# Kernel tuning notes

Hardware: AMD Instinct MI355X
Metric: run time of the kernel (lower is better)

The kernel has to match this reference:

```python
import jax, jax.numpy as jnp
import numpy as np

D_MODEL = 1024
NUM_HEADS = 16
HEAD_DIM = D_MODEL // NUM_HEADS
SCALE = HEAD_DIM ** -0.5
LN_EPS = 1e-5
Q_EPS = 1e-5


def bit_quant(W):
    # BitNet b1.58 ternary weight quantization with straight-through estimator.
    gamma = jnp.mean(jnp.abs(W))
    Wq = jnp.clip(jnp.round(W / (gamma + Q_EPS)), -1.0, 1.0) * gamma
    return W + jax.lax.stop_gradient(Wq - W)


def layer_norm(x, gamma, beta):
    mu = jnp.mean(x, axis=-1, keepdims=True)
    var = jnp.mean(jnp.square(x - mu), axis=-1, keepdims=True)
    return (x - mu) * jax.lax.rsqrt(var + LN_EPS) * gamma + beta


def setup_inputs() -> dict:
    key = jax.random.key(0)
    ks = jax.random.split(key, 8)
    B, T, T_ctx, C = 4, 1024, 2048, D_MODEL
    w_std = C ** -0.5
    return {
        "x": jax.random.normal(ks[0], (B, T, C), jnp.float32),
        "context": jax.random.normal(ks[1], (B, T_ctx, C), jnp.float32),
        "Wq": jax.random.normal(ks[2], (C, C), jnp.float32) * w_std,
        "bq": jnp.zeros((C,), jnp.float32),
        "Wk": jax.random.normal(ks[3], (C, C), jnp.float32) * w_std,
        "bk": jnp.zeros((C,), jnp.float32),
        "Wv": jax.random.normal(ks[4], (C, C), jnp.float32) * w_std,
        "bv": jnp.zeros((C,), jnp.float32),
        "Wo": jax.random.normal(ks[5], (C, C), jnp.float32) * w_std,
        "bo": jnp.zeros((C,), jnp.float32),
        "ln_gamma": jnp.ones((C,), jnp.float32),
        "ln_beta": jnp.zeros((C,), jnp.float32),
    }


def reference(x, context, Wq, bq, Wk, bk, Wv, bv, Wo, bo, ln_gamma, ln_beta):
    B, T, C = x.shape
    T_ctx = context.shape[1]
    residual = x
    xn = layer_norm(x, ln_gamma, ln_beta)
    # BitNet-quantized projections (torch Linear: y = x @ W.T + b)
    q = xn @ bit_quant(Wq).T + bq                      # [B,T,C]
    k = context @ bit_quant(Wk).T + bk                 # [B,T_ctx,C]
    v = context @ bit_quant(Wv).T + bv                 # [B,T_ctx,C]
    q = q.reshape(B, T, NUM_HEADS, HEAD_DIM)
    k = k.reshape(B, T_ctx, NUM_HEADS, HEAD_DIM)
    v = v.reshape(B, T_ctx, NUM_HEADS, HEAD_DIM)
    scores = jnp.einsum("bqhd,bkhd->bhqk", q, k) * SCALE   # [B,H,T,T_ctx]
    probs = jax.nn.softmax(scores, axis=-1)
    out = jnp.einsum("bhqk,bkhd->bqhd", probs, v).reshape(B, T, C)
    return residual + (out @ bit_quant(Wo).T + bo)
```

## Files before the change

### kernel.cpp

```cpp
#include <hip/hip_runtime.h>
#include <hip/hip_bf16.h>

typedef __attribute__((ext_vector_type(8))) short s8x;
typedef __attribute__((ext_vector_type(4))) float f4x;
typedef unsigned short u16;
typedef unsigned int u32;

#define T_ 1024
#define TC_ 2048

__device__ __forceinline__ u16 f2bf(float f) {
    u32 u = __float_as_uint(f);
    return (u16)((u + 0x7fffu + ((u >> 16) & 1u)) >> 16);
}

#if defined(__has_builtin)
#if __has_builtin(__builtin_amdgcn_cvt_pk_bf16_f32)
#define HAVE_PK 1
#endif
#endif

__device__ __forceinline__ u32 pack2bf(float a, float b) {
#ifdef HAVE_PK
    typedef __attribute__((ext_vector_type(2))) __bf16 bf2t;
    bf2t r = __builtin_amdgcn_cvt_pk_bf16_f32(a, b);
    u32 u;
    __builtin_memcpy(&u, &r, 4);
    return u;
#else
    return (u32)f2bf(a) | ((u32)f2bf(b) << 16);
#endif
}

__device__ __forceinline__ void gload16(const void* g, void* l) {
    __builtin_amdgcn_global_load_lds((const __attribute__((address_space(1))) u32*)g,
                                     (__attribute__((address_space(3))) u32*)l, 16, 0, 0);
}

__global__ __launch_bounds__(256) void absmean_k(const float* __restrict__ W0, const float* __restrict__ W1,
                                                 const float* __restrict__ W2, const float* __restrict__ W3,
                                                 float* __restrict__ gsum) {
    int wi = blockIdx.y;
    const float* W = (wi == 0) ? W0 : (wi == 1) ? W1 : (wi == 2) ? W2 : W3;
    const int n4 = (1024 * 1024) / 4;
    float s = 0.f;
    int stride = gridDim.x * blockDim.x;
    for (int i = blockIdx.x * blockDim.x + threadIdx.x; i < n4; i += stride) {
        float4 v = ((const float4*)W)[i];
        s += fabsf(v.x) + fabsf(v.y) + fabsf(v.z) + fabsf(v.w);
    }
#pragma unroll
    for (int off = 32; off; off >>= 1) s += __shfl_down(s, off, 64);
    __shared__ float ps[4];
    if ((threadIdx.x & 63) == 0) ps[threadIdx.x >> 6] = s;
    __syncthreads();
    if (threadIdx.x == 0) atomicAdd(gsum + wi, ps[0] + ps[1] + ps[2] + ps[3]);
}

__global__ __launch_bounds__(256) void prep_k(
        const float* __restrict__ x, const float* __restrict__ lng, const float* __restrict__ lnb,
        u16* __restrict__ xn,
        const float* __restrict__ ctx, u16* __restrict__ ctxb,
        const float* __restrict__ W0, const float* __restrict__ W1,
        const float* __restrict__ W2, const float* __restrict__ W3,
        u16* __restrict__ D0, u16* __restrict__ D1, u16* __restrict__ D2, u16* __restrict__ D3,
        const float* __restrict__ gsum) {
    __shared__ float ps[8];
    int bx = blockIdx.x, t = threadIdx.x;
    if (bx < 4096) {
        int row = bx;
        float4 xv = ((const float4*)(x + (long)row * 1024))[t];
        float s = xv.x + xv.y + xv.z + xv.w;
        float s2 = xv.x * xv.x + xv.y * xv.y + xv.z * xv.z + xv.w * xv.w;
#pragma unroll
        for (int off = 32; off; off >>= 1) { s += __shfl_down(s, off, 64); s2 += __shfl_down(s2, off, 64); }
        if ((t & 63) == 0) { ps[t >> 6] = s; ps[4 + (t >> 6)] = s2; }
        __syncthreads();
        float S = ps[0] + ps[1] + ps[2] + ps[3];
        float S2 = ps[4] + ps[5] + ps[6] + ps[7];
        float mu = S * (1.f / 1024.f);
        float var = S2 * (1.f / 1024.f) - mu * mu;
        float rstd = rsqrtf(var + 1e-5f);
        float4 gv = ((const float4*)lng)[t];
        float4 bv = ((const float4*)lnb)[t];
        uint2 o;
        o.x = pack2bf((xv.x - mu) * rstd * gv.x + bv.x, (xv.y - mu) * rstd * gv.y + bv.y);
        o.y = pack2bf((xv.z - mu) * rstd * gv.z + bv.z, (xv.w - mu) * rstd * gv.w + bv.w);
        ((uint2*)(xn + (long)row * 1024))[t] = o;
    } else if (bx < 12288) {
        int i = (bx - 4096) * 256 + t;
        float4 v = ((const float4*)ctx)[i];
        uint2 o = {pack2bf(v.x, v.y), pack2bf(v.z, v.w)};
        ((uint2*)ctxb)[i] = o;
    } else {
        int wi = (bx - 12288) >> 10;
        const float* W = (wi == 0) ? W0 : (wi == 1) ? W1 : (wi == 2) ? W2 : W3;
        u16* D = (wi == 0) ? D0 : (wi == 1) ? D1 : (wi == 2) ? D2 : D3;
        float inv = 1.0f / (gsum[wi] * (1.0f / 1048576.0f) + 1e-5f);
        int i = ((bx - 12288) & 1023) * 256 + t;
        float4 wv = ((const float4*)W)[i];
        uint2 o;
        o.x = pack2bf(fminf(1.f, fmaxf(-1.f, rintf(wv.x * inv))),
                      fminf(1.f, fmaxf(-1.f, rintf(wv.y * inv))));
        o.y = pack2bf(fminf(1.f, fmaxf(-1.f, rintf(wv.z * inv))),
                      fminf(1.f, fmaxf(-1.f, rintf(wv.w * inv))));
        ((uint2*)D)[i] = o;
    }
}

__global__ __launch_bounds__(256) void gemm_fused(
        const u16* __restrict__ xn, const u16* __restrict__ ctxb,
        const u16* __restrict__ wtq, const u16* __restrict__ wtk, const u16* __restrict__ wtv,
        const float* __restrict__ bq, const float* __restrict__ bk, const float* __restrict__ bv,
        const float* __restrict__ gsum,
        u16* __restrict__ qb, u16* __restrict__ kb, u16* __restrict__ vtb) {
    __shared__ __align__(16) char smem[32768];
    int tid = threadIdx.x;
    int w = tid >> 6, l = tid & 63, lq = l & 15, lh = l >> 4;
    int wm = (w >> 1) * 64, wn = (w & 1) * 64;
    int bx = blockIdx.x;
    int prob; const u16 *A, *Wt; const float* bias; int tshift; float sc; int gidx;
    if (bx < 256)      { prob = 0;            A = xn;   Wt = wtq; bias = bq; tshift = 10; sc = 0.125f; gidx = 0; }
    else if (bx < 768) { prob = 1; bx -= 256; A = ctxb; Wt = wtk; bias = bk; tshift = 11; sc = 1.0f;  gidx = 1; }
    else               { prob = 2; bx -= 768; A = ctxb; Wt = wtv; bias = bv; tshift = 11; sc = 1.0f;  gidx = 2; }
    int m0 = (bx >> 3) * 128, n0 = (bx & 7) * 128;
    char* AsB = smem;
    char* BsB = smem + 16384;
    f4x acc[4][4] = {};
    int rb = tid >> 3;
    int cg = (tid & 7) ^ (rb & 7);
    const u16* Ag = A + (long)m0 * 1024 + cg * 8;
    const u16* Bg = Wt + (long)n0 * 1024 + cg * 8;
    for (int k0 = 0; k0 < 1024; k0 += 64) {
        __syncthreads();
#pragma unroll
        for (int i = 0; i < 4; i++) {
            gload16(Ag + (long)(i * 32 + rb) * 1024 + k0, AsB + (i * 256 + tid) * 16);
            gload16(Bg + (long)(i * 32 + rb) * 1024 + k0, BsB + (i * 256 + tid) * 16);
        }
        __syncthreads();
#pragma unroll
        for (int s = 0; s < 2; s++) {
            int sl = (s * 4 + lh) ^ (lq & 7);
            s8x af[4], bfr[4];
#pragma unroll
            for (int i = 0; i < 4; i++) {
                af[i] = *(const s8x*)(AsB + (wm + i * 16 + lq) * 128 + sl * 16);
                bfr[i] = *(const s8x*)(BsB + (wn + i * 16 + lq) * 128 + sl * 16);
            }
#pragma unroll
            for (int i = 0; i < 4; i++)
#pragma unroll
                for (int j = 0; j < 4; j++)
                    acc[i][j] = __builtin_amdgcn_mfma_f32_16x16x32_bf16(af[i], bfr[j], acc[i][j], 0, 0, 0);
        }
    }
    float gamma = gsum[gidx] * (1.0f / 1048576.0f) * sc;
    if (prob < 2) {
        u16* outq = (prob == 0) ? qb : kb;
        int tmask = (1 << tshift) - 1;
#pragma unroll
        for (int i = 0; i < 4; i++) {
            int gr = m0 + wm + i * 16 + lh * 4;
#pragma unroll
            for (int j = 0; j < 4; j++) {
                int gc = n0 + wn + j * 16 + lq;
                float bb = bias[gc] * sc;
                int h = gc >> 6, d = gc & 63;
#pragma unroll
                for (int r = 0; r < 4; r++) {
                    int row = gr + r;
                    int bidx = row >> tshift, tt = row & tmask;
                    outq[((((long)(bidx * 16 + h)) << tshift) + tt) * 64 + d] = f2bf(acc[i][j][r] * gamma + bb);
                }
            }
        }
    } else {
        __syncthreads();
        char* Ct = smem;
#pragma unroll
        for (int i = 0; i < 4; i++) {
            int tt = wm + i * 16 + lh * 4;
#pragma unroll
            for (int j = 0; j < 4; j++) {
                int c = wn + j * 16 + lq;
                float bb = bias[n0 + c];
                uint2 pk;
                pk.x = pack2bf(acc[i][j][0] * gamma + bb, acc[i][j][1] * gamma + bb);
                pk.y = pack2bf(acc[i][j][2] * gamma + bb, acc[i][j][3] * gamma + bb);
                int slot = (tt >> 3) ^ (c & 15);
                *(uint2*)(Ct + c * 256 + slot * 16 + (tt & 7) * 2) = pk;
            }
        }
        __syncthreads();
        int b = m0 >> 11, t0 = m0 & 2047;
#pragma unroll
        for (int it = 0; it < 8; it++) {
            int e = it * 256 + tid;
            int c = e >> 4, ch = e & 15;
            int slot = ch ^ (c & 15);
            s8x v = *(const s8x*)(Ct + c * 256 + slot * 16);
            int gcg = n0 + c;
            int h = gcg >> 6, d = gcg & 63;
            *(s8x*)(vtb + ((long)((b * 16 + h) * 64 + d)) * TC_ + t0 + ch * 8) = v;
        }
    }
}

__global__ __launch_bounds__(256) void gemm_o(const u16* __restrict__ A, const u16* __restrict__ Wt,
                                              const float* __restrict__ bias, const float* __restrict__ gsum,
                                              const float* __restrict__ residual, float* __restrict__ outr) {
    __shared__ __align__(16) char smem[24576];
    int tid = threadIdx.x;
    int w = tid >> 6, l = tid & 63, lq = l & 15, lh = l >> 4;
    int wm = (w >> 1) * 64, wn = (w & 1) * 32;
    int bx = blockIdx.x;
    int m0 = (bx >> 4) * 128, n0 = (bx & 15) * 64;
    char* AsB = smem;
    char* BsB = smem + 16384;
    f4x acc[4][2] = {};
    int rb = tid >> 3;
    int cg = (tid & 7) ^ (rb & 7);
    const u16* Ag = A + (long)m0 * 1024 + cg * 8;
    const u16* Bg = Wt + (long)n0 * 1024 + cg * 8;
    for (int k0 = 0; k0 < 1024; k0 += 64) {
        __syncthreads();
#pragma unroll
        for (int i = 0; i < 4; i++)
            gload16(Ag + (long)(i * 32 + rb) * 1024 + k0, AsB + (i * 256 + tid) * 16);
#pragma unroll
        for (int i = 0; i < 2; i++)
            gload16(Bg + (long)(i * 32 + rb) * 1024 + k0, BsB + (i * 256 + tid) * 16);
        __syncthreads();
#pragma unroll
        for (int s = 0; s < 2; s++) {
            int sl = (s * 4 + lh) ^ (lq & 7);
            s8x af[4], bfr[2];
#pragma unroll
            for (int i = 0; i < 4; i++)
                af[i] = *(const s8x*)(AsB + (wm + i * 16 + lq) * 128 + sl * 16);
#pragma unroll
            for (int j = 0; j < 2; j++)
                bfr[j] = *(const s8x*)(BsB + (wn + j * 16 + lq) * 128 + sl * 16);
#pragma unroll
            for (int i = 0; i < 4; i++)
#pragma unroll
                for (int j = 0; j < 2; j++)
                    acc[i][j] = __builtin_amdgcn_mfma_f32_16x16x32_bf16(af[i], bfr[j], acc[i][j], 0, 0, 0);
        }
    }
    float gamma = gsum[3] * (1.0f / 1048576.0f);
#pragma unroll
    for (int i = 0; i < 4; i++) {
        int gr = m0 + wm + i * 16 + lh * 4;
#pragma unroll
        for (int j = 0; j < 2; j++) {
            int gc = n0 + wn + j * 16 + lq;
            float bb = bias[gc];
#pragma unroll
            for (int r = 0; r < 4; r++) {
                long idx = (long)(gr + r) * 1024 + gc;
                outr[idx] = residual[idx] + acc[i][j][r] * gamma + bb;
            }
        }
    }
}

__global__ __launch_bounds__(256) void attn_k(const u16* __restrict__ qh, const u16* __restrict__ kh,
                                              const u16* __restrict__ vth, u16* __restrict__ attn) {
    __shared__ __align__(16) char smem[51200];
    int tid = threadIdx.x, w = tid >> 6, l = tid & 63, lq = l & 15, lh = l >> 4;
    int bh = blockIdx.x, q0 = blockIdx.y * 128;
    const u16* qp = qh + ((long)bh * T_ + q0) * 64;
    const u16* kp = kh + (long)bh * TC_ * 64;
    const u16* vp = vth + (long)bh * 64 * TC_;
#pragma unroll
    for (int i = 0; i < 4; i++) {
        int cid = i * 256 + tid;
        int r = cid >> 3, c = (cid & 7) ^ (r & 7);
        gload16(qp + r * 64 + c * 8, smem + cid * 16);
    }
    __syncthreads();
    s8x qf[2][2];
#pragma unroll
    for (int nb = 0; nb < 2; nb++)
#pragma unroll
        for (int dh = 0; dh < 2; dh++) {
            int qrow = w * 32 + nb * 16 + lq;
            int ch = (dh * 4 + lh) ^ (qrow & 7);
            qf[nb][dh] = *(const s8x*)(smem + qrow * 128 + ch * 16);
        }
    __syncthreads();
#define STAGE_KV(kt, buf)                                                          \
    {                                                                              \
        char* Kb = smem + (buf) * 16384;                                           \
        char* Vb = Kb + 8192;                                                      \
        _Pragma("unroll") for (int i = 0; i < 2; i++) {                            \
            int cid = i * 256 + tid;                                               \
            int r = cid >> 3, c = (cid & 7) ^ (r & 7);                             \
            gload16(kp + ((kt) * 64 + r) * 64 + c * 8, Kb + cid * 16);             \
            gload16(vp + (long)r * TC_ + (kt) * 64 + c * 8, Vb + cid * 16);        \
        }                                                                          \
    }
    STAGE_KV(0, 0);
    f4x oacc[2][4] = {};
    f4x lrun[2] = {};
    float mrun = -1e30f;
    const s8x ones = {16256, 16256, 16256, 16256, 16256, 16256, 16256, 16256};
    char* Psb = smem + 32768 + w * 4608;
    for (int kt = 0; kt < TC_ / 64; kt++) {
        __syncthreads();
        if (kt + 1 < TC_ / 64) STAGE_KV(kt + 1, (kt + 1) & 1);
        char* Ksb = smem + (kt & 1) * 16384;
        char* Vsb = Ksb + 8192;
        f4x z[2][4];
#pragma unroll
        for (int ni = 0; ni < 4; ni++) {
            int kr = ni * 16 + lq;
            s8x a0 = *(const s8x*)(Ksb + kr * 128 + ((lh) ^ (kr & 7)) * 16);
            s8x a1 = *(const s8x*)(Ksb + kr * 128 + ((4 + lh) ^ (kr & 7)) * 16);
#pragma unroll
            for (int nb = 0; nb < 2; nb++) {
                f4x zz = {0.f, 0.f, 0.f, 0.f};
                zz = __builtin_amdgcn_mfma_f32_16x16x32_bf16(a0, qf[nb][0], zz, 0, 0, 0);
                zz = __builtin_amdgcn_mfma_f32_16x16x32_bf16(a1, qf[nb][1], zz, 0, 0, 0);
                z[nb][ni] = zz;
            }
        }
        float mx = -1e30f;
#pragma unroll
        for (int nb = 0; nb < 2; nb++)
#pragma unroll
            for (int ni = 0; ni < 4; ni++)
#pragma unroll
                for (int r = 0; r < 4; r++) mx = fmaxf(mx, z[nb][ni][r]);
#pragma unroll
        for (int s = 1; s <= 32; s <<= 1) mx = fmaxf(mx, __shfl_xor(mx, s));
        float mn = fmaxf(mrun, mx);
        float al = __expf(mrun - mn);
        mrun = mn;
#pragma unroll
        for (int nb = 0; nb < 2; nb++) {
            int prow = nb * 16 + lq;
#pragma unroll
            for (int ni = 0; ni < 4; ni++) {
                uint2 pk;
                pk.x = pack2bf(__expf(z[nb][ni][0] - mn), __expf(z[nb][ni][1] - mn));
                pk.y = pack2bf(__expf(z[nb][ni][2] - mn), __expf(z[nb][ni][3] - mn));
                *(uint2*)(Psb + prow * 144 + ni * 32 + lh * 8) = pk;
            }
        }
        if (al != 1.0f) {
#pragma unroll
            for (int qb = 0; qb < 2; qb++) {
#pragma unroll
                for (int nd = 0; nd < 4; nd++)
#pragma unroll
                    for (int r = 0; r < 4; r++) oacc[qb][nd][r] *= al;
#pragma unroll
                for (int r = 0; r < 4; r++) lrun[qb][r] *= al;
            }
        }
        s8x vf[4][2];
#pragma unroll
        for (int nd = 0; nd < 4; nd++) {
            int vr = nd * 16 + lq;
            vf[nd][0] = *(const s8x*)(Vsb + vr * 128 + ((lh) ^ (vr & 7)) * 16);
            vf[nd][1] = *(const s8x*)(Vsb + vr * 128 + ((4 + lh) ^ (vr & 7)) * 16);
        }
#pragma unroll
        for (int qb = 0; qb < 2; qb++) {
            int prow = qb * 16 + lq;
            s8x pf0 = *(const s8x*)(Psb + prow * 144 + lh * 16);
            s8x pf1 = *(const s8x*)(Psb + prow * 144 + 64 + lh * 16);
            f4x rs = {0.f, 0.f, 0.f, 0.f};
            rs = __builtin_amdgcn_mfma_f32_16x16x32_bf16(pf0, ones, rs, 0, 0, 0);
            rs = __builtin_amdgcn_mfma_f32_16x16x32_bf16(pf1, ones, rs, 0, 0, 0);
#pragma unroll
            for (int r = 0; r < 4; r++) lrun[qb][r] += rs[r];
#pragma unroll
            for (int nd = 0; nd < 4; nd++) {
                oacc[qb][nd] = __builtin_amdgcn_mfma_f32_16x16x32_bf16(pf0, vf[nd][0], oacc[qb][nd], 0, 0, 0);
                oacc[qb][nd] = __builtin_amdgcn_mfma_f32_16x16x32_bf16(pf1, vf[nd][1], oacc[qb][nd], 0, 0, 0);
            }
        }
    }
    int b = bh >> 4, h = bh & 15;
#pragma unroll
    for (int qb = 0; qb < 2; qb++)
#pragma unroll
        for (int r = 0; r < 4; r++) {
            int q = q0 + w * 32 + qb * 16 + lh * 4 + r;
            float rcp = 1.f / lrun[qb][r];
#pragma unroll
            for (int nd = 0; nd < 4; nd++)
                attn[((long)(b * T_ + q)) * 1024 + h * 64 + nd * 16 + lq] = f2bf(oacc[qb][nd][r] * rcp);
        }
}

extern "C" void kernel_launch(void* const* d_in, const int* in_sizes, int n_in,
                              void* d_out, int out_size, void* d_ws, size_t ws_size,
                              hipStream_t stream) {
    const float* x   = (const float*)d_in[0];
    const float* ctx = (const float*)d_in[1];
    const float* Wq  = (const float*)d_in[2];
    const float* bq  = (const float*)d_in[3];
    const float* Wk  = (const float*)d_in[4];
    const float* bk  = (const float*)d_in[5];
    const float* Wv  = (const float*)d_in[6];
    const float* bv  = (const float*)d_in[7];
    const float* Wo  = (const float*)d_in[8];
    const float* bo  = (const float*)d_in[9];
    const float* lng = (const float*)d_in[10];
    const float* lnb = (const float*)d_in[11];
    float* out = (float*)d_out;

    char* ws = (char*)d_ws;
    float* gsum = (float*)ws;
    size_t off = 256;
    u16* wtq  = (u16*)(ws + off); off += (size_t)1024 * 1024 * 2;
    u16* wtk  = (u16*)(ws + off); off += (size_t)1024 * 1024 * 2;
    u16* wtv  = (u16*)(ws + off); off += (size_t)1024 * 1024 * 2;
    u16* wto  = (u16*)(ws + off); off += (size_t)1024 * 1024 * 2;
    u16* ctxb = (u16*)(ws + off); off += (size_t)8192 * 1024 * 2;
    u16* xn   = (u16*)(ws + off); off += (size_t)4096 * 1024 * 2;
    u16* qb_  = (u16*)(ws + off); off += (size_t)4096 * 1024 * 2;
    u16* kb   = (u16*)(ws + off); off += (size_t)8192 * 1024 * 2;
    u16* vtb  = (u16*)(ws + off); off += (size_t)8192 * 1024 * 2;
    u16* attnb = xn;

    hipMemsetAsync(gsum, 0, 16, stream);
    absmean_k<<<dim3(128, 4), 256, 0, stream>>>(Wq, Wk, Wv, Wo, gsum);
    prep_k<<<16384, 256, 0, stream>>>(x, lng, lnb, xn, ctx, ctxb,
                                      Wq, Wk, Wv, Wo, wtq, wtk, wtv, wto, gsum);
    gemm_fused<<<1280, 256, 0, stream>>>(xn, ctxb, wtq, wtk, wtv, bq, bk, bv, gsum, qb_, kb, vtb);
    attn_k<<<dim3(64, 8), 256, 0, stream>>>(qb_, kb, vtb, attnb);
    gemm_o<<<512, 256, 0, stream>>>(attnb, wto, bo, gsum, x, out);
}
```

Measured before the change: 281.8 us.

## Split attention block across 8 waves with 16 query rows each, use exp2

The attention kernel now launches 512 threads per block. Each of the 8 waves handles 16 query rows instead of 32, which halves per-wave registers and the P scratch and gives the scheduler more waves to hide latency. The K/V staging loads are spread over twice as many threads. The log2(e) factor is folded into the Q projection scale so the softmax can use the native exp2 instruction. In exchange, each K/V tile is reused by fewer query rows per wave, so there are more LDS reads of K and V per unit of MFMA work.

Result: faster. 274.9 us (-2.5%).

```diff
diff --git a/kernel.cpp b/kernel.cpp
--- a/kernel.cpp
+++ b/kernel.cpp
@@ -8,6 +8,7 @@
 
 #define T_ 1024
 #define TC_ 2048
+#define SCLOG2E 0.1803368801111243f
 
 __device__ __forceinline__ u16 f2bf(float f) {
     u32 u = __float_as_uint(f);
@@ -120,7 +121,7 @@
     int wm = (w >> 1) * 64, wn = (w & 1) * 64;
     int bx = blockIdx.x;
     int prob; const u16 *A, *Wt; const float* bias; int tshift; float sc; int gidx;
-    if (bx < 256)      { prob = 0;            A = xn;   Wt = wtq; bias = bq; tshift = 10; sc = 0.125f; gidx = 0; }
+    if (bx < 256)      { prob = 0;            A = xn;   Wt = wtq; bias = bq; tshift = 10; sc = SCLOG2E; gidx = 0; }
     else if (bx < 768) { prob = 1; bx -= 256; A = ctxb; Wt = wtk; bias = bk; tshift = 11; sc = 1.0f;  gidx = 1; }
     else               { prob = 2; bx -= 768; A = ctxb; Wt = wtv; bias = bv; tshift = 11; sc = 1.0f;  gidx = 2; }
     int m0 = (bx >> 3) * 128, n0 = (bx & 7) * 128;
@@ -266,7 +267,7 @@
     }
 }
 
-__global__ __launch_bounds__(256) void attn_k(const u16* __restrict__ qh, const u16* __restrict__ kh,
+__global__ __launch_bounds__(512) void attn_k(const u16* __restrict__ qh, const u16* __restrict__ kh,
                                               const u16* __restrict__ vth, u16* __restrict__ attn) {
     __shared__ __align__(16) char smem[51200];
     int tid = threadIdx.x, w = tid >> 6, l = tid & 63, lq = l & 15, lh = l >> 4;
@@ -275,127 +276,102 @@
     const u16* kp = kh + (long)bh * TC_ * 64;
     const u16* vp = vth + (long)bh * 64 * TC_;
 #pragma unroll
-    for (int i = 0; i < 4; i++) {
-        int cid = i * 256 + tid;
+    for (int i = 0; i < 2; i++) {
+        int cid = i * 512 + tid;
         int r = cid >> 3, c = (cid & 7) ^ (r & 7);
         gload16(qp + r * 64 + c * 8, smem + cid * 16);
     }
     __syncthreads();
-    s8x qf[2][2];
-#pragma unroll
-    for (int nb = 0; nb < 2; nb++)
-#pragma unroll
-        for (int dh = 0; dh < 2; dh++) {
-            int qrow = w * 32 + nb * 16 + lq;
-            int ch = (dh * 4 + lh) ^ (qrow & 7);
-            qf[nb][dh] = *(const s8x*)(smem + qrow * 128 + ch * 16);
-        }
+    s8x qf0, qf1;
+    {
+        int qrow = w * 16 + lq;
+        qf0 = *(const s8x*)(smem + qrow * 128 + ((lh) ^ (qrow & 7)) * 16);
+        qf1 = *(const s8x*)(smem + qrow * 128 + ((4 + lh) ^ (qrow & 7)) * 16);
+    }
     __syncthreads();
-#define STAGE_KV(kt, buf)                                                          \
-    {                                                                              \
-        char* Kb = smem + (buf) * 16384;                                           \
-        char* Vb = Kb + 8192;                                                      \
-        _Pragma("unroll") for (int i = 0; i < 2; i++) {                            \
-            int cid = i * 256 + tid;                                               \
-            int r = cid >> 3, c = (cid & 7) ^ (r & 7);                             \
-            gload16(kp + ((kt) * 64 + r) * 64 + c * 8, Kb + cid * 16);             \
-            gload16(vp + (long)r * TC_ + (kt) * 64 + c * 8, Vb + cid * 16);        \
-        }                                                                          \
+#define STAGE_KV(kt, buf)                                                      \
+    {                                                                          \
+        char* Kb = smem + (buf) * 16384;                                       \
+        char* Vb = Kb + 8192;                                                  \
+        int r = tid >> 3, c = (tid & 7) ^ (r & 7);                             \
+        gload16(kp + ((kt) * 64 + r) * 64 + c * 8, Kb + tid * 16);             \
+        gload16(vp + (long)r * TC_ + (kt) * 64 + c * 8, Vb + tid * 16);        \
     }
     STAGE_KV(0, 0);
-    f4x oacc[2][4] = {};
-    f4x lrun[2] = {};
+    f4x oacc[4] = {};
+    f4x lrun = {};
     float mrun = -1e30f;
     const s8x ones = {16256, 16256, 16256, 16256, 16256, 16256, 16256, 16256};
-    char* Psb = smem + 32768 + w * 4608;
+    char* Psb = smem + 32768 + w * 2304;
     for (int kt = 0; kt < TC_ / 64; kt++) {
         __syncthreads();
         if (kt + 1 < TC_ / 64) STAGE_KV(kt + 1, (kt + 1) & 1);
         char* Ksb = smem + (kt & 1) * 16384;
         char* Vsb = Ksb + 8192;
-        f4x z[2][4];
+        f4x z[4];
 #pragma unroll
         for (int ni = 0; ni < 4; ni++) {
             int kr = ni * 16 + lq;
             s8x a0 = *(const s8x*)(Ksb + kr * 128 + ((lh) ^ (kr & 7)) * 16);
             s8x a1 = *(const s8x*)(Ksb + kr * 128 + ((4 + lh) ^ (kr & 7)) * 16);
-#pragma unroll
-            for (int nb = 0; nb < 2; nb++) {
-                f4x zz = {0.f, 0.f, 0.f, 0.f};
-                zz = __builtin_amdgcn_mfma_f32_16x16x32_bf16(a0, qf[nb][0], zz, 0, 0, 0);
-                zz = __builtin_amdgcn_mfma_f32_16x16x32_bf16(a1, qf[nb][1], zz, 0, 0, 0);
-                z[nb][ni] = zz;
-            }
-        }
-        float mx = -1e30f;
-#pragma unroll
-        for (int nb = 0; nb < 2; nb++)
-#pragma unroll
-            for (int ni = 0; ni < 4; ni++)
-#pragma unroll
-                for (int r = 0; r < 4; r++) mx = fmaxf(mx, z[nb][ni][r]);
+            f4x zz = {0.f, 0.f, 0.f, 0.f};
+            zz = __builtin_amdgcn_mfma_f32_16x16x32_bf16(a0, qf0, zz, 0, 0, 0);
+            zz = __builtin_amdgcn_mfma_f32_16x16x32_bf16(a1, qf1, zz, 0, 0, 0);
+            z[ni] = zz;
+        }
+        float mx = fmaxf(fmaxf(fmaxf(z[0][0], z[0][1]), fmaxf(z[0][2], z[0][3])),
+                         fmaxf(fmaxf(z[1][0], z[1][1]), fmaxf(z[1][2], z[1][3])));
+        mx = fmaxf(mx, fmaxf(fmaxf(fmaxf(z[2][0], z[2][1]), fmaxf(z[2][2], z[2][3])),
+                             fmaxf(fmaxf(z[3][0], z[3][1]), fmaxf(z[3][2], z[3][3]))));
 #pragma unroll
         for (int s = 1; s <= 32; s <<= 1) mx = fmaxf(mx, __shfl_xor(mx, s));
         float mn = fmaxf(mrun, mx);
-        float al = __expf(mrun - mn);
+        float al = __builtin_amdgcn_exp2f(mrun - mn);
         mrun = mn;
 #pragma unroll
-        for (int nb = 0; nb < 2; nb++) {
-            int prow = nb * 16 + lq;
-#pragma unroll
-            for (int ni = 0; ni < 4; ni++) {
-                uint2 pk;
-                pk.x = pack2bf(__expf(z[nb][ni][0] - mn), __expf(z[nb][ni][1] - mn));
-                pk.y = pack2bf(__expf(z[nb][ni][2] - mn), __expf(z[nb][ni][3] - mn));
-                *(uint2*)(Psb + prow * 144 + ni * 32 + lh * 8) = pk;
-            }
+        for (int ni = 0; ni < 4; ni++) {
+            uint2 pk;
+            pk.x = pack2bf(__builtin_amdgcn_exp2f(z[ni][0] - mn), __builtin_amdgcn_exp2f(z[ni][1] - mn));
+            pk.y = pack2bf(__builtin_amdgcn_exp2f(z[ni][2] - mn), __builtin_amdgcn_exp2f(z[ni][3] - mn));
+            *(uint2*)(Psb + lq * 144 + ni * 32 + lh * 8) = pk;
         }
         if (al != 1.0f) {
 #pragma unroll
-            for (int qb = 0; qb < 2; qb++) {
-#pragma unroll
-                for (int nd = 0; nd < 4; nd++)
-#pragma unroll
-                    for (int r = 0; r < 4; r++) oacc[qb][nd][r] *= al;
-#pragma unroll
-                for (int r = 0; r < 4; r++) lrun[qb][r] *= al;
-            }
-        }
-        s8x vf[4][2];
+            for (int nd = 0; nd < 4; nd++)
+#pragma unroll
+                for (int r = 0; r < 4; r++) oacc[nd][r] *= al;
+#pragma unroll
+            for (int r = 0; r < 4; r++) lrun[r] *= al;
+        }
+        s8x vf0[4], vf1[4];
 #pragma unroll
         for (int nd = 0; nd < 4; nd++) {
             int vr = nd * 16 + lq;
-            vf[nd][0] = *(const s8x*)(Vsb + vr * 128 + ((lh) ^ (vr & 7)) * 16);
-            vf[nd][1] = *(const s8x*)(Vsb + vr * 128 + ((4 + lh) ^ (vr & 7)) * 16);
-        }
-#pragma unroll
-        for (int qb = 0; qb < 2; qb++) {
-            int prow = qb * 16 + lq;
-            s8x pf0 = *(const s8x*)(Psb + prow * 144 + lh * 16);
-            s8x pf1 = *(const s8x*)(Psb + prow * 144 + 64 + lh * 16);
-            f4x rs = {0.f, 0.f, 0.f, 0.f};
-            rs = __builtin_amdgcn_mfma_f32_16x16x32_bf16(pf0, ones, rs, 0, 0, 0);
-            rs = __builtin_amdgcn_mfma_f32_16x16x32_bf16(pf1, ones, rs, 0, 0, 0);
-#pragma unroll
-            for (int r = 0; r < 4; r++) lrun[qb][r] += rs[r];
-#pragma unroll
-            for (int nd = 0; nd < 4; nd++) {
-                oacc[qb][nd] = __builtin_amdgcn_mfma_f32_16x16x32_bf16(pf0, vf[nd][0], oacc[qb][nd], 0, 0, 0);
-                oacc[qb][nd] = __builtin_amdgcn_mfma_f32_16x16x32_bf16(pf1, vf[nd][1], oacc[qb][nd], 0, 0, 0);
-            }
+            vf0[nd] = *(const s8x*)(Vsb + vr * 128 + ((lh) ^ (vr & 7)) * 16);
+            vf1[nd] = *(const s8x*)(Vsb + vr * 128 + ((4 + lh) ^ (vr & 7)) * 16);
+        }
+        s8x pf0 = *(const s8x*)(Psb + lq * 144 + lh * 16);
+        s8x pf1 = *(const s8x*)(Psb + lq * 144 + 64 + lh * 16);
+        f4x rs = {0.f, 0.f, 0.f, 0.f};
+        rs = __builtin_amdgcn_mfma_f32_16x16x32_bf16(pf0, ones, rs, 0, 0, 0);
+        rs = __builtin_amdgcn_mfma_f32_16x16x32_bf16(pf1, ones, rs, 0, 0, 0);
+#pragma unroll
+        for (int r = 0; r < 4; r++) lrun[r] += rs[r];
+#pragma unroll
+        for (int nd = 0; nd < 4; nd++) {
+            oacc[nd] = __builtin_amdgcn_mfma_f32_16x16x32_bf16(pf0, vf0[nd], oacc[nd], 0, 0, 0);
+            oacc[nd] = __builtin_amdgcn_mfma_f32_16x16x32_bf16(pf1, vf1[nd], oacc[nd], 0, 0, 0);
         }
     }
     int b = bh >> 4, h = bh & 15;
 #pragma unroll
-    for (int qb = 0; qb < 2; qb++)
-#pragma unroll
-        for (int r = 0; r < 4; r++) {
-            int q = q0 + w * 32 + qb * 16 + lh * 4 + r;
-            float rcp = 1.f / lrun[qb][r];
-#pragma unroll
-            for (int nd = 0; nd < 4; nd++)
-                attn[((long)(b * T_ + q)) * 1024 + h * 64 + nd * 16 + lq] = f2bf(oacc[qb][nd][r] * rcp);
-        }
+    for (int r = 0; r < 4; r++) {
+        int q = q0 + w * 16 + lh * 4 + r;
+        float rcp = 1.f / lrun[r];
+#pragma unroll
+        for (int nd = 0; nd < 4; nd++)
+            attn[((long)(b * T_ + q)) * 1024 + h * 64 + nd * 16 + lq] = f2bf(oacc[nd][r] * rcp);
+    }
 }
 
 extern "C" void kernel_launch(void* const* d_in, const int* in_sizes, int n_in,
@@ -434,6 +410,6 @@
     prep_k<<<16384, 256, 0, stream>>>(x, lng, lnb, xn, ctx, ctxb,
                                       Wq, Wk, Wv, Wo, wtq, wtk, wtv, wto, gsum);
     gemm_fused<<<1280, 256, 0, stream>>>(xn, ctxb, wtq, wtk, wtv, bq, bk, bv, gsum, qb_, kb, vtb);
-    attn_k<<<dim3(64, 8), 256, 0, stream>>>(qb_, kb, vtb, attnb);
+    attn_k<<<dim3(64, 8), 512, 0, stream>>>(qb_, kb, vtb, attnb);
     gemm_o<<<512, 256, 0, stream>>>(attnb, wto, bo, gsum, x, out);
 }
```
